# Optimization experiments

Measured on AMD Instinct MI355X. Metric: run time of the kernel, lower is better.

Reference implementation:

```python
import jax, jax.numpy as jnp
import numpy as np

N, F_IN, HID, C, H = 4096, 1024, 64, 40, 8
ALPHA = 0.2  # LeakyReLU negative slope
NEG_INF = -9e15

def setup_inputs() -> dict:
    key = jax.random.key(0)
    ks = jax.random.split(key, 8)
    x = jax.random.normal(ks[0], (N, F_IN), jnp.float32)
    adj = jax.random.randint(ks[1], (N, N), 0, 2, jnp.int32)  # dense 0/1 adjacency
    W = jax.random.normal(ks[2], (H, F_IN, HID), jnp.float32) / np.sqrt(F_IN).astype(np.float32)
    a_src = jax.random.normal(ks[3], (H, HID), jnp.float32) * 0.1
    a_dst = jax.random.normal(ks[4], (H, HID), jnp.float32) * 0.1
    W_out = jax.random.normal(ks[5], (H * HID, C), jnp.float32) / np.sqrt(H * HID).astype(np.float32)
    ao_src = jax.random.normal(ks[6], (C,), jnp.float32) * 0.1
    ao_dst = jax.random.normal(ks[7], (C,), jnp.float32) * 0.1
    return dict(x=x, adj=adj, W=W, a_src=a_src, a_dst=a_dst,
                W_out=W_out, ao_src=ao_src, ao_dst=ao_dst)

def _masked_attention(src, dst, mask):
    # src: [..., N] scores for row node i; dst: [..., N] scores for col node j
    e = jax.nn.leaky_relu(src[..., :, None] + dst[..., None, :], ALPHA)  # [..., N, N]
    e = jnp.where(mask, e, NEG_INF)
    return jax.nn.softmax(e, axis=-1)

def reference(x, adj, W, a_src, a_dst, W_out, ao_src, ao_dst):
    mask = adj > 0  # [N, N]
    # multi-head GAT layer (concat=True)
    Wh = jnp.einsum('nf,hfo->hno', x, W)            # [H, N, HID]
    src = jnp.einsum('hno,ho->hn', Wh, a_src)       # [H, N]
    dst = jnp.einsum('hno,ho->hn', Wh, a_dst)       # [H, N]
    att = _masked_attention(src, dst, mask[None])   # [H, N, N]
    h = jnp.einsum('hij,hjo->hio', att, Wh)         # [H, N, HID]
    h = jax.nn.elu(h)                               # concat=True -> elu inside layer
    h = jnp.transpose(h, (1, 0, 2)).reshape(N, H * HID)  # concat heads -> [N, H*HID]
    # output GAT layer (concat=False -> no elu inside)
    Wh2 = h @ W_out                                 # [N, C]
    att2 = _masked_attention(Wh2 @ ao_src, Wh2 @ ao_dst, mask)  # [N, N]
    out = att2 @ Wh2                                # [N, C]
    # model-level: elu then log_softmax over classes
    return jax.nn.log_softmax(jax.nn.elu(out), axis=1)
```

## Files before the change

kernel.cpp:

```cpp
#include <hip/hip_runtime.h>

#define NN 4096
#define F_IN 1024
#define NHEAD 8
#define HID 64
#define NCLS 40
#define LOG2E 1.44269504f

typedef float f32x4 __attribute__((ext_vector_type(4)));
typedef float f32x2 __attribute__((ext_vector_type(2)));
typedef short s16x8 __attribute__((ext_vector_type(8)));

#define SWZ(r,c) (((r)*64) + ((c) ^ (((r)&7)<<3)))

__device__ __forceinline__ unsigned short f2bf(float f){
  unsigned u = __float_as_uint(f);
  return (unsigned short)((u + 0x7fffu + ((u >> 16) & 1u)) >> 16);
}
__device__ __forceinline__ unsigned cvtpk(float lo, float hi){
  unsigned r; asm("v_cvt_pk_bf16_f32 %0, %1, %2" : "=v"(r) : "v"(lo), "v"(hi)); return r;
}
__device__ __forceinline__ f32x2 pkmul(f32x2 a, f32x2 b){
  f32x2 r; asm("v_pk_mul_f32 %0, %1, %2" : "=v"(r) : "v"(a), "v"(b)); return r;
}

__global__ __launch_bounds__(256) void pack_adj_k(const int* __restrict__ adj, unsigned* __restrict__ bmT){
  int gid = blockIdx.x*256 + threadIdx.x;
  int lane = threadIdx.x & 63;
  unsigned long long m = __ballot(adj[gid] > 0);
  int w = gid >> 5, i = w >> 7, jw = w & 127;
  if (lane == 0)       bmT[(size_t)jw*NN + i] = (unsigned)m;
  else if (lane == 32) bmT[(size_t)jw*NN + i] = (unsigned)(m >> 32);
}

__global__ __launch_bounds__(256) void cast_W_k(const float* __restrict__ W, unsigned short* __restrict__ WbT){
  __shared__ float T[64][65];
  const int h = blockIdx.y, k0 = blockIdx.x*64, t = threadIdx.x;
  for (int idx = t; idx < 1024; idx += 256){
    int k = idx >> 4, c4 = idx & 15;
    *(float4*)&T[k][c4*4] = *(const float4*)&W[((size_t)h*F_IN + k0 + k)*HID + c4*4];
  }
  __syncthreads();
  for (int idx = t; idx < 512; idx += 256){
    int o = idx >> 3, ch = idx & 7;
    s16x8 v;
    #pragma unroll
    for (int e = 0; e < 8; ++e) v[e] = (short)f2bf(T[ch*8 + e][o]);
    *(s16x8*)&WbT[((size_t)h*HID + o)*F_IN + k0 + ch*8] = v;
  }
}

__global__ __launch_bounds__(256) void cast_Wo_k(const float* __restrict__ Wout, unsigned short* __restrict__ WoT){
  int idx = blockIdx.x*256 + threadIdx.x;
  int cc = idx >> 9, k = idx & 511;
  WoT[idx] = (cc < NCLS) ? f2bf(Wout[(size_t)k*NCLS + cc]) : (unsigned short)0;
}

__global__ __launch_bounds__(256) void gemm1_k(const float* __restrict__ x,
    const unsigned short* __restrict__ WbT, unsigned short* __restrict__ WhT,
    const float* __restrict__ a_src, const float* __restrict__ a_dst,
    float* __restrict__ srcv, float* __restrict__ dstv, float2* __restrict__ bdv){
  __shared__ unsigned short xS[64*64];
  __shared__ unsigned short wS[64*64];
  const int t = threadIdx.x, l = t & 63, wv = t >> 6, g = l >> 4, c = l & 15;
  const int h = blockIdx.y, n0 = blockIdx.x * 64;
  f32x4 acc[4] = {};
  for (int k0 = 0; k0 < F_IN; k0 += 64){
    __syncthreads();
    #pragma unroll
    for (int p = 0; p < 4; ++p){
      int idx = t + p*256, row = idx >> 4, c4 = idx & 15;
      float4 v = *(const float4*)&x[(size_t)(n0+row)*F_IN + k0 + c4*4];
      *(uint2*)&xS[SWZ(row, c4*4)] = make_uint2(cvtpk(v.x, v.y), cvtpk(v.z, v.w));
    }
    #pragma unroll
    for (int p = 0; p < 2; ++p){
      int idx = t + p*256, o = idx >> 3, ch = idx & 7;
      *(s16x8*)&wS[SWZ(o, ch*8)] = *(const s16x8*)&WbT[(size_t)(h*HID + o)*F_IN + k0 + ch*8];
    }
    __syncthreads();
    #pragma unroll
    for (int ks = 0; ks < 2; ++ks){
      s16x8 av = *(const s16x8*)&xS[SWZ(wv*16 + c, ks*32 + g*8)];
      #pragma unroll
      for (int ct = 0; ct < 4; ++ct){
        s16x8 bv = *(const s16x8*)&wS[SWZ(ct*16 + c, ks*32 + g*8)];
        acc[ct] = __builtin_amdgcn_mfma_f32_16x16x32_bf16(av, bv, acc[ct], 0, 0, 0);
      }
    }
  }
  float asv[4], adv[4];
  #pragma unroll
  for (int ct = 0; ct < 4; ++ct){ asv[ct] = a_src[h*HID + ct*16 + c]; adv[ct] = a_dst[h*HID + ct*16 + c]; }
  #pragma unroll
  for (int r = 0; r < 4; ++r){
    float ps = acc[0][r]*asv[0] + acc[1][r]*asv[1] + acc[2][r]*asv[2] + acc[3][r]*asv[3];
    float pd = acc[0][r]*adv[0] + acc[1][r]*adv[1] + acc[2][r]*adv[2] + acc[3][r]*adv[3];
    #pragma unroll
    for (int off = 1; off < 16; off <<= 1){ ps += __shfl_xor(ps, off); pd += __shfl_xor(pd, off); }
    if (c == 0){
      int n = n0 + wv*16 + g*4 + r;
      srcv[h*NN + n] = ps; dstv[h*NN + n] = pd;
      bdv[h*NN + n] = make_float2(exp2f(pd*LOG2E), exp2f(0.2f*pd*LOG2E));
    }
  }
  __syncthreads();
  #pragma unroll
  for (int ct = 0; ct < 4; ++ct)
    *(uint2*)&xS[SWZ(ct*16 + c, wv*16 + g*4)] = make_uint2(cvtpk(acc[ct][0], acc[ct][1]), cvtpk(acc[ct][2], acc[ct][3]));
  __syncthreads();
  #pragma unroll
  for (int p = 0; p < 2; ++p){
    int idx = t + p*256, o = idx >> 3, ch = idx & 7;
    *(s16x8*)&WhT[(size_t)(h*HID + o)*NN + n0 + ch*8] = *(const s16x8*)&xS[SWZ(o, ch*8)];
  }
}

__global__ __launch_bounds__(256) void maxred_k(const float* __restrict__ in, float* __restrict__ out){
  __shared__ float red[4];
  const float* p = in + (size_t)blockIdx.x*NN;
  float m = -3.0e38f;
  for (int i = threadIdx.x; i < NN; i += 256) m = fmaxf(m, p[i]);
  #pragma unroll
  for (int off = 32; off; off >>= 1) m = fmaxf(m, __shfl_xor(m, off));
  if ((threadIdx.x & 63) == 0) red[threadIdx.x >> 6] = m;
  __syncthreads();
  if (threadIdx.x == 0) out[blockIdx.x] = fmaxf(fmaxf(red[0], red[1]), fmaxf(red[2], red[3]));
}

template<int NCT, int NJT, int MODE>
__global__ __launch_bounds__(256) void agg_mfma_k(
    const unsigned* __restrict__ bmT, const unsigned short* __restrict__ VT,
    const float* __restrict__ srcv, const float2* __restrict__ bdv,
    const float* __restrict__ maxp, float* __restrict__ partOut, float* __restrict__ denOut)
{
  __shared__ unsigned short vS[2][2][NCT*16*64];
  __shared__ float2 dS[2][2][64];
  __shared__ unsigned bitS[2][2][2][32];
  const int t = threadIdx.x, l = t & 63, wv = t >> 6, g = l >> 4, c = l & 15;
  const int h  = (MODE == 0) ? (blockIdx.y >> 1) : 0;
  const int ck = (MODE == 0) ? (blockIdx.y & 1)  : blockIdx.y;
  const int jt0 = ck * NJT;
  const int i0 = blockIdx.x * 32;
  const int tl = wv >> 1, rH = wv & 1;
  const int lr = rH*16 + c;
  const float sr = srcv[h*NN + i0 + lr];
  const float mx = maxp[MODE == 0 ? h : 0];
  const float tm = sr + mx;
  const float mi2 = fmaxf(tm, 0.2f*tm) * LOG2E;
  f32x2 ac2;
  ac2[0] = exp2f(fmaf(sr, LOG2E, -mi2));
  ac2[1] = exp2f(fmaf(0.2f*sr, LOG2E, -mi2));
  const unsigned short* vb = VT + (MODE == 0 ? (size_t)h*HID*NN : (size_t)0);
  const float2* bp = bdv + (MODE == 0 ? (size_t)h*NN : (size_t)0);

  f32x4 acc[NCT] = {};
  f32x4 accs = {};
  s16x8 ones;
  #pragma unroll
  for (int e = 0; e < 8; ++e) ones[e] = (short)0x3F80;

  s16x8 vreg[NCT]; float2 dreg = make_float2(0.f, 0.f); unsigned breg = 0;
  auto loadRegs = [&](int jt){
    #pragma unroll
    for (int p = 0; p < NCT; ++p){
      int u = t + p*256;
      int tt = u / (NCT*128), rem = u % (NCT*128);
      int o = rem >> 3, chk = rem & 7;
      vreg[p] = *(const s16x8*)&vb[(size_t)o*NN + (jt+tt)*64 + chk*8];
    }
    if (t < 128){
      f32x2 bd = *(const f32x2*)&bp[(jt + (t>>6))*64 + (t&63)];
      dreg = make_float2(bd[0], bd[1]);
    }
    else { int u = t - 128; breg = bmT[(size_t)((jt + (u>>6))*2 + ((u>>5)&1))*NN + i0 + (u&31)]; }
  };
  auto writeLDS = [&](int b){
    #pragma unroll
    for (int p = 0; p < NCT; ++p){
      int u = t + p*256;
      int tt = u / (NCT*128), rem = u % (NCT*128);
      int o = rem >> 3, chk = rem & 7;
      *(s16x8*)&vS[b][tt][SWZ(o, chk*8)] = vreg[p];
    }
    if (t < 128) dS[b][t>>6][t&63] = dreg;
    else { int u = t - 128; bitS[b][u>>6][(u>>5)&1][u&31] = breg; }
  };
  auto computeBuf = [&](int b){
    #pragma unroll
    for (int ks = 0; ks < 2; ++ks){
      unsigned wb = (bitS[b][tl][ks][lr] >> (g*8)) & 0xffu;
      const f32x2* dr = (const f32x2*)&dS[b][tl][ks*32 + g*8];
      float q[8];
      #pragma unroll
      for (int e = 0; e < 8; ++e){
        f32x2 pr = pkmul(ac2, dr[e]);
        float m3 = __builtin_amdgcn_fmed3f(pr[0], pr[1], 1.0f);
        q[e] = (wb & (1u << e)) ? m3 : 0.f;
      }
      s16x8 afr;
      ((unsigned*)&afr)[0] = cvtpk(q[0], q[1]);
      ((unsigned*)&afr)[1] = cvtpk(q[2], q[3]);
      ((unsigned*)&afr)[2] = cvtpk(q[4], q[5]);
      ((unsigned*)&afr)[3] = cvtpk(q[6], q[7]);
      #pragma unroll
      for (int ct = 0; ct < NCT; ++ct){
        s16x8 bv = *(const s16x8*)&vS[b][tl][SWZ(ct*16 + c, ks*32 + g*8)];
        acc[ct] = __builtin_amdgcn_mfma_f32_16x16x32_bf16(afr, bv, acc[ct], 0, 0, 0);
      }
      accs = __builtin_amdgcn_mfma_f32_16x16x32_bf16(afr, ones, accs, 0, 0, 0);
    }
  };

  loadRegs(jt0);
  writeLDS(0);
  __syncthreads();
  int cur = 0;
  for (int jj = 0; jj < NJT; jj += 2){
    const bool more = (jj + 2 < NJT);
    if (more) loadRegs(jt0 + jj + 2);
    computeBuf(cur);
    if (more) writeLDS(cur ^ 1);
    __syncthreads();
    cur ^= 1;
  }

  float* mrg = (float*)&vS[0][0][0];
  constexpr int S = (NCT + 1) * 4;
  if (tl == 1){
    int base = (rH*64 + l) * S;
    #pragma unroll
    for (int ct = 0; ct < NCT; ++ct)
      #pragma unroll
      for (int r = 0; r < 4; ++r) mrg[base + ct*4 + r] = acc[ct][r];
    #pragma unroll
    for (int r = 0; r < 4; ++r) mrg[base + NCT*4 + r] = accs[r];
  }
  __syncthreads();
  if (tl == 0){
    int base = (rH*64 + l) * S;
    #pragma unroll
    for (int ct = 0; ct < NCT; ++ct)
      #pragma unroll
      for (int r = 0; r < 4; ++r) acc[ct][r] += mrg[base + ct*4 + r];
    #pragma unroll
    for (int r = 0; r < 4; ++r) accs[r] += mrg[base + NCT*4 + r];
    if (MODE == 0){
      float* ob = partOut + (size_t)ck * NN * (NHEAD*HID);
      #pragma unroll
      for (int r = 0; r < 4; ++r){
        int row = i0 + rH*16 + g*4 + r;
        #pragma unroll
        for (int ct = 0; ct < NCT; ++ct)
          ob[(size_t)row*(NHEAD*HID) + h*HID + ct*16 + c] = acc[ct][r];
        if (c == 0) denOut[(size_t)(ck*NHEAD + h)*NN + row] = accs[r];
      }
    } else {
      float* ob = partOut + (size_t)ck * NN * 64;
      #pragma unroll
      for (int r = 0; r < 4; ++r){
        int row = i0 + rH*16 + g*4 + r;
        #pragma unroll
        for (int ct = 0; ct < NCT; ++ct)
          ob[(size_t)row*64 + ct*16 + c] = acc[ct][r];
        if (c == 0) ob[(size_t)row*64 + 48] = accs[r];
      }
    }
  }
}

__global__ __launch_bounds__(256) void merge1_k(const float* __restrict__ part, const float* __restrict__ den,
                                                unsigned short* __restrict__ hb){
  int idx = blockIdx.x*256 + threadIdx.x;
  int row = idx >> 7, q = idx & 127;
  float4 a = *(const float4*)&part[(size_t)row*(NHEAD*HID) + q*4];
  float4 b = *(const float4*)&part[((size_t)NN + row)*(NHEAD*HID) + q*4];
  int h = q >> 4;
  float dn = den[(size_t)h*NN + row] + den[(size_t)(NHEAD + h)*NN + row];
  float inv = 1.f / fmaxf(dn, 1e-30f);
  float v0 = (a.x + b.x)*inv, v1 = (a.y + b.y)*inv, v2 = (a.z + b.z)*inv, v3 = (a.w + b.w)*inv;
  v0 = v0 > 0.f ? v0 : __expf(v0) - 1.f;
  v1 = v1 > 0.f ? v1 : __expf(v1) - 1.f;
  v2 = v2 > 0.f ? v2 : __expf(v2) - 1.f;
  v3 = v3 > 0.f ? v3 : __expf(v3) - 1.f;
  *(uint2*)&hb[(size_t)row*(NHEAD*HID) + q*4] = make_uint2(cvtpk(v0, v1), cvtpk(v2, v3));
}

__global__ __launch_bounds__(256) void gemm2_k(const unsigned short* __restrict__ hb,
    const unsigned short* __restrict__ WoT, const float* __restrict__ aos, const float* __restrict__ aod,
    unsigned short* __restrict__ WhT2, float* __restrict__ s2, float* __restrict__ d2,
    float2* __restrict__ bd2){
  __shared__ unsigned short aS[64*64];
  __shared__ unsigned short bS[48*64];
  const int t = threadIdx.x, l = t & 63, wv = t >> 6, g = l >> 4, c = l & 15;
  const int n0 = blockIdx.x * 64;
  f32x4 acc[3] = {};
  for (int k0 = 0; k0 < NHEAD*HID; k0 += 64){
    __syncthreads();
    #pragma unroll
    for (int p = 0; p < 2; ++p){
      int u = t + p*256, o = u >> 3, ch = u & 7;
      *(s16x8*)&aS[SWZ(o, ch*8)] = *(const s16x8*)&hb[(size_t)(n0+o)*(NHEAD*HID) + k0 + ch*8];
    }
    for (int u = t; u < 384; u += 256){
      int o = u >> 3, ch = u & 7;
      *(s16x8*)&bS[SWZ(o, ch*8)] = *(const s16x8*)&WoT[(size_t)o*(NHEAD*HID) + k0 + ch*8];
    }
    __syncthreads();
    #pragma unroll
    for (int ks = 0; ks < 2; ++ks){
      s16x8 av = *(const s16x8*)&aS[SWZ(wv*16 + c, ks*32 + g*8)];
      #pragma unroll
      for (int ct = 0; ct < 3; ++ct){
        s16x8 bv = *(const s16x8*)&bS[SWZ(ct*16 + c, ks*32 + g*8)];
        acc[ct] = __builtin_amdgcn_mfma_f32_16x16x32_bf16(av, bv, acc[ct], 0, 0, 0);
      }
    }
  }
  float asv[3], adv[3];
  #pragma unroll
  for (int ct = 0; ct < 3; ++ct){
    int col = ct*16 + c;
    asv[ct] = (col < NCLS) ? aos[col] : 0.f;
    adv[ct] = (col < NCLS) ? aod[col] : 0.f;
  }
  #pragma unroll
  for (int r = 0; r < 4; ++r){
    float ps = acc[0][r]*asv[0] + acc[1][r]*asv[1] + acc[2][r]*asv[2];
    float pd = acc[0][r]*adv[0] + acc[1][r]*adv[1] + acc[2][r]*adv[2];
    #pragma unroll
    for (int off = 1; off < 16; off <<= 1){ ps += __shfl_xor(ps, off); pd += __shfl_xor(pd, off); }
    if (c == 0){
      int n = n0 + wv*16 + g*4 + r;
      s2[n] = ps; d2[n] = pd;
      bd2[n] = make_float2(exp2f(pd*LOG2E), exp2f(0.2f*pd*LOG2E));
    }
  }
  __syncthreads();
  #pragma unroll
  for (int ct = 0; ct < 3; ++ct)
    *(uint2*)&bS[SWZ(ct*16 + c, wv*16 + g*4)] = make_uint2(cvtpk(acc[ct][0], acc[ct][1]), cvtpk(acc[ct][2], acc[ct][3]));
  __syncthreads();
  for (int u = t; u < 384; u += 256){
    int o = u >> 3, ch = u & 7;
    *(s16x8*)&WhT2[(size_t)o*NN + n0 + ch*8] = *(const s16x8*)&bS[SWZ(o, ch*8)];
  }
}

__global__ __launch_bounds__(256) void final_k(const float* __restrict__ part, float* __restrict__ out){
  const int wid = (blockIdx.x*256 + threadIdx.x) >> 6;
  const int c = threadIdx.x & 63;
  float acc = 0.f, rs = 0.f;
  #pragma unroll
  for (int ch = 0; ch < 8; ++ch){
    const float* pb = part + ((size_t)ch*NN + wid)*64;
    if (c < 48) acc += pb[c];
    rs += pb[48];
  }
  float v = acc / fmaxf(rs, 1e-30f);
  float e = v > 0.f ? v : __expf(v) - 1.f;
  float ev = (c < NCLS) ? e : -3.0e38f;
  float m = ev;
  #pragma unroll
  for (int off = 32; off; off >>= 1) m = fmaxf(m, __shfl_xor(m, off));
  float ex = (c < NCLS) ? __expf(e - m) : 0.f;
  float s = ex;
  #pragma unroll
  for (int off = 32; off; off >>= 1) s += __shfl_xor(s, off);
  if (c < NCLS) out[(size_t)wid*NCLS + c] = e - m - __logf(s);
}

extern "C" void kernel_launch(void* const* d_in, const int* in_sizes, int n_in,
                              void* d_out, int out_size, void* d_ws, size_t ws_size,
                              hipStream_t stream){
  (void)in_sizes; (void)n_in; (void)out_size; (void)ws_size;
  const float* x     = (const float*)d_in[0];
  const int*   adj   = (const int*)  d_in[1];
  const float* W     = (const float*)d_in[2];
  const float* a_src = (const float*)d_in[3];
  const float* a_dst = (const float*)d_in[4];
  const float* W_out = (const float*)d_in[5];
  const float* aos   = (const float*)d_in[6];
  const float* aod   = (const float*)d_in[7];
  float* out = (float*)d_out;

  char* p = (char*)d_ws;
  unsigned* bmT        = (unsigned*)p;       p += (size_t)NN*128*4;
  unsigned short* WbT  = (unsigned short*)p; p += (size_t)NHEAD*HID*F_IN*2;
  unsigned short* WhT  = (unsigned short*)p; p += (size_t)NHEAD*HID*NN*2;
  unsigned short* hbuf = (unsigned short*)p; p += (size_t)NN*NHEAD*HID*2;
  unsigned short* WoT  = (unsigned short*)p; p += (size_t)48*NHEAD*HID*2;
  unsigned short* WhT2 = (unsigned short*)p; p += (size_t)48*NN*2;
  float* srcv = (float*)p; p += (size_t)NHEAD*NN*4;
  float* dstv = (float*)p; p += (size_t)NHEAD*NN*4;
  float* maxd = (float*)p; p += 256;
  float* s2   = (float*)p; p += (size_t)NN*4;
  float* d2   = (float*)p; p += (size_t)NN*4;
  float* m2   = (float*)p; p += 256;
  float2* bdv1 = (float2*)p; p += (size_t)NHEAD*NN*8;
  float2* bdv2 = (float2*)p; p += (size_t)NN*8;
  float* den1 = (float*)p; p += (size_t)2*NHEAD*NN*4;
  float* partU = (float*)p; p += (size_t)2*NN*NHEAD*HID*4;

  pack_adj_k<<<(NN*NN)/256, 256, 0, stream>>>(adj, bmT);
  cast_W_k<<<dim3(F_IN/64, NHEAD), 256, 0, stream>>>(W, WbT);
  cast_Wo_k<<<96, 256, 0, stream>>>(W_out, WoT);
  gemm1_k<<<dim3(NN/64, NHEAD), 256, 0, stream>>>(x, WbT, WhT, a_src, a_dst, srcv, dstv, bdv1);
  maxred_k<<<NHEAD, 256, 0, stream>>>(dstv, maxd);
  agg_mfma_k<4, 32, 0><<<dim3(NN/32, 16), 256, 0, stream>>>(bmT, WhT, srcv, bdv1, maxd, partU, den1);
  merge1_k<<<(NN*128)/256, 256, 0, stream>>>(partU, den1, hbuf);
  gemm2_k<<<NN/64, 256, 0, stream>>>(hbuf, WoT, aos, aod, WhT2, s2, d2, bdv2);
  maxred_k<<<1, 256, 0, stream>>>(d2, m2);
  agg_mfma_k<3, 8, 1><<<dim3(NN/32, 8), 256, 0, stream>>>(bmT, WhT2, s2, bdv2, m2, partU, nullptr);
  final_k<<<NN/4, 256, 0, stream>>>(partU, out);
}
```

Measured before the change: 162.0 us.

## Retile attention aggregation to 64-row blocks with more j-chunks and bf16 partials

The aggregation kernel now gives each block 64 rows, with every wave owning 16 rows across the full j-tile. This replaces the two-wave j-split and removes the LDS merge step at the end. The j dimension is split into more chunks (4 for layer one, 16 for layer two), and layer-one partials are stored as bf16 to cut merge traffic. Launch bounds request higher occupancy and per-block LDS shrinks. The trade-offs are more partial sums for the merge and final kernels to read, and bf16 rounding of the unnormalized partial accumulators.

```diff
diff --git a/kernel.cpp b/kernel.cpp
--- a/kernel.cpp
+++ b/kernel.cpp
@@ -16,6 +16,9 @@
 __device__ __forceinline__ unsigned short f2bf(float f){
   unsigned u = __float_as_uint(f);
   return (unsigned short)((u + 0x7fffu + ((u >> 16) & 1u)) >> 16);
+}
+__device__ __forceinline__ float bf2f(unsigned short u){
+  return __uint_as_float((unsigned)u << 16);
 }
 __device__ __forceinline__ unsigned cvtpk(float lo, float hi){
   unsigned r; asm("v_cvt_pk_bf16_f32 %0, %1, %2" : "=v"(r) : "v"(lo), "v"(hi)); return r;
@@ -129,21 +132,20 @@
 }
 
 template<int NCT, int NJT, int MODE>
-__global__ __launch_bounds__(256) void agg_mfma_k(
+__global__ __launch_bounds__(256, 8) void agg_mfma_k(
     const unsigned* __restrict__ bmT, const unsigned short* __restrict__ VT,
     const float* __restrict__ srcv, const float2* __restrict__ bdv,
-    const float* __restrict__ maxp, float* __restrict__ partOut, float* __restrict__ denOut)
+    const float* __restrict__ maxp, void* __restrict__ partOut, float* __restrict__ denOut)
 {
-  __shared__ unsigned short vS[2][2][NCT*16*64];
-  __shared__ float2 dS[2][2][64];
-  __shared__ unsigned bitS[2][2][2][32];
+  __shared__ unsigned short vS[2][NCT*16*64];
+  __shared__ float2 dS[2][64];
+  __shared__ unsigned bitS[2][2][64];
   const int t = threadIdx.x, l = t & 63, wv = t >> 6, g = l >> 4, c = l & 15;
-  const int h  = (MODE == 0) ? (blockIdx.y >> 1) : 0;
-  const int ck = (MODE == 0) ? (blockIdx.y & 1)  : blockIdx.y;
+  const int h  = (MODE == 0) ? (blockIdx.y >> 2) : 0;
+  const int ck = (MODE == 0) ? (blockIdx.y & 3)  : blockIdx.y;
   const int jt0 = ck * NJT;
-  const int i0 = blockIdx.x * 32;
-  const int tl = wv >> 1, rH = wv & 1;
-  const int lr = rH*16 + c;
+  const int i0 = blockIdx.x * 64;
+  const int lr = wv*16 + c;
   const float sr = srcv[h*NN + i0 + lr];
   const float mx = maxp[MODE == 0 ? h : 0];
   const float tm = sr + mx;
@@ -160,37 +162,36 @@
   #pragma unroll
   for (int e = 0; e < 8; ++e) ones[e] = (short)0x3F80;
 
-  s16x8 vreg[NCT]; float2 dreg = make_float2(0.f, 0.f); unsigned breg = 0;
+  s16x8 vreg[2]; float2 dreg = make_float2(0.f, 0.f); unsigned breg = 0;
   auto loadRegs = [&](int jt){
     #pragma unroll
-    for (int p = 0; p < NCT; ++p){
+    for (int p = 0; p < 2; ++p){
       int u = t + p*256;
-      int tt = u / (NCT*128), rem = u % (NCT*128);
-      int o = rem >> 3, chk = rem & 7;
-      vreg[p] = *(const s16x8*)&vb[(size_t)o*NN + (jt+tt)*64 + chk*8];
-    }
-    if (t < 128){
-      f32x2 bd = *(const f32x2*)&bp[(jt + (t>>6))*64 + (t&63)];
-      dreg = make_float2(bd[0], bd[1]);
-    }
-    else { int u = t - 128; breg = bmT[(size_t)((jt + (u>>6))*2 + ((u>>5)&1))*NN + i0 + (u&31)]; }
+      if (u < NCT*128){
+        int o = u >> 3, chk = u & 7;
+        vreg[p] = *(const s16x8*)&vb[(size_t)o*NN + jt*64 + chk*8];
+      }
+    }
+    if (t < 64) { f32x2 bd = *(const f32x2*)&bp[jt*64 + t]; dreg = make_float2(bd[0], bd[1]); }
+    else if (t < 192){ int u = t - 64; breg = bmT[(size_t)(jt*2 + (u>>6))*NN + i0 + (u & 63)]; }
   };
   auto writeLDS = [&](int b){
     #pragma unroll
-    for (int p = 0; p < NCT; ++p){
+    for (int p = 0; p < 2; ++p){
       int u = t + p*256;
-      int tt = u / (NCT*128), rem = u % (NCT*128);
-      int o = rem >> 3, chk = rem & 7;
-      *(s16x8*)&vS[b][tt][SWZ(o, chk*8)] = vreg[p];
-    }
-    if (t < 128) dS[b][t>>6][t&63] = dreg;
-    else { int u = t - 128; bitS[b][u>>6][(u>>5)&1][u&31] = breg; }
+      if (u < NCT*128){
+        int o = u >> 3, chk = u & 7;
+        *(s16x8*)&vS[b][SWZ(o, chk*8)] = vreg[p];
+      }
+    }
+    if (t < 64) dS[b][t] = dreg;
+    else if (t < 192){ int u = t - 64; bitS[b][u>>6][u&63] = breg; }
   };
   auto computeBuf = [&](int b){
     #pragma unroll
     for (int ks = 0; ks < 2; ++ks){
-      unsigned wb = (bitS[b][tl][ks][lr] >> (g*8)) & 0xffu;
-      const f32x2* dr = (const f32x2*)&dS[b][tl][ks*32 + g*8];
+      unsigned wb = (bitS[b][ks][lr] >> (g*8)) & 0xffu;
+      const f32x2* dr = (const f32x2*)&dS[b][ks*32 + g*8];
       float q[8];
       #pragma unroll
       for (int e = 0; e < 8; ++e){
@@ -205,7 +206,7 @@
       ((unsigned*)&afr)[3] = cvtpk(q[6], q[7]);
       #pragma unroll
       for (int ct = 0; ct < NCT; ++ct){
-        s16x8 bv = *(const s16x8*)&vS[b][tl][SWZ(ct*16 + c, ks*32 + g*8)];
+        s16x8 bv = *(const s16x8*)&vS[b][SWZ(ct*16 + c, ks*32 + g*8)];
         acc[ct] = __builtin_amdgcn_mfma_f32_16x16x32_bf16(afr, bv, acc[ct], 0, 0, 0);
       }
       accs = __builtin_amdgcn_mfma_f32_16x16x32_bf16(afr, ones, accs, 0, 0, 0);
@@ -216,74 +217,60 @@
   writeLDS(0);
   __syncthreads();
   int cur = 0;
-  for (int jj = 0; jj < NJT; jj += 2){
-    const bool more = (jj + 2 < NJT);
-    if (more) loadRegs(jt0 + jj + 2);
+  for (int jj = 0; jj < NJT; ++jj){
+    const bool more = (jj + 1 < NJT);
+    if (more) loadRegs(jt0 + jj + 1);
     computeBuf(cur);
     if (more) writeLDS(cur ^ 1);
     __syncthreads();
     cur ^= 1;
   }
 
-  float* mrg = (float*)&vS[0][0][0];
-  constexpr int S = (NCT + 1) * 4;
-  if (tl == 1){
-    int base = (rH*64 + l) * S;
-    #pragma unroll
-    for (int ct = 0; ct < NCT; ++ct)
-      #pragma unroll
-      for (int r = 0; r < 4; ++r) mrg[base + ct*4 + r] = acc[ct][r];
-    #pragma unroll
-    for (int r = 0; r < 4; ++r) mrg[base + NCT*4 + r] = accs[r];
-  }
-  __syncthreads();
-  if (tl == 0){
-    int base = (rH*64 + l) * S;
-    #pragma unroll
-    for (int ct = 0; ct < NCT; ++ct)
-      #pragma unroll
-      for (int r = 0; r < 4; ++r) acc[ct][r] += mrg[base + ct*4 + r];
-    #pragma unroll
-    for (int r = 0; r < 4; ++r) accs[r] += mrg[base + NCT*4 + r];
-    if (MODE == 0){
-      float* ob = partOut + (size_t)ck * NN * (NHEAD*HID);
-      #pragma unroll
-      for (int r = 0; r < 4; ++r){
-        int row = i0 + rH*16 + g*4 + r;
-        #pragma unroll
-        for (int ct = 0; ct < NCT; ++ct)
-          ob[(size_t)row*(NHEAD*HID) + h*HID + ct*16 + c] = acc[ct][r];
-        if (c == 0) denOut[(size_t)(ck*NHEAD + h)*NN + row] = accs[r];
-      }
-    } else {
-      float* ob = partOut + (size_t)ck * NN * 64;
-      #pragma unroll
-      for (int r = 0; r < 4; ++r){
-        int row = i0 + rH*16 + g*4 + r;
-        #pragma unroll
-        for (int ct = 0; ct < NCT; ++ct)
-          ob[(size_t)row*64 + ct*16 + c] = acc[ct][r];
-        if (c == 0) ob[(size_t)row*64 + 48] = accs[r];
-      }
-    }
-  }
-}
-
-__global__ __launch_bounds__(256) void merge1_k(const float* __restrict__ part, const float* __restrict__ den,
+  if (MODE == 0){
+    unsigned short* ob = (unsigned short*)partOut + (size_t)ck * NN * (NHEAD*HID);
+    #pragma unroll
+    for (int r = 0; r < 4; ++r){
+      int row = i0 + wv*16 + g*4 + r;
+      #pragma unroll
+      for (int ct = 0; ct < NCT; ++ct)
+        ob[(size_t)row*(NHEAD*HID) + h*HID + ct*16 + c] = f2bf(acc[ct][r]);
+      if (c == 0) denOut[(size_t)(ck*NHEAD + h)*NN + row] = accs[r];
+    }
+  } else {
+    float* ob = (float*)partOut + (size_t)ck * NN * 64;
+    #pragma unroll
+    for (int r = 0; r < 4; ++r){
+      int row = i0 + wv*16 + g*4 + r;
+      #pragma unroll
+      for (int ct = 0; ct < NCT; ++ct)
+        ob[(size_t)row*64 + ct*16 + c] = acc[ct][r];
+      if (c == 0) ob[(size_t)row*64 + 48] = accs[r];
+    }
+  }
+}
+
+__global__ __launch_bounds__(256) void merge1_k(const unsigned short* __restrict__ part,
+                                                const float* __restrict__ den,
                                                 unsigned short* __restrict__ hb){
   int idx = blockIdx.x*256 + threadIdx.x;
   int row = idx >> 7, q = idx & 127;
-  float4 a = *(const float4*)&part[(size_t)row*(NHEAD*HID) + q*4];
-  float4 b = *(const float4*)&part[((size_t)NN + row)*(NHEAD*HID) + q*4];
   int h = q >> 4;
-  float dn = den[(size_t)h*NN + row] + den[(size_t)(NHEAD + h)*NN + row];
+  float v[4] = {0.f, 0.f, 0.f, 0.f};
+  float dn = 0.f;
+  #pragma unroll
+  for (int ck = 0; ck < 4; ++ck){
+    const unsigned short* pb = part + ((size_t)ck*NN + row)*(NHEAD*HID) + q*4;
+    ushort4 u = *(const ushort4*)pb;
+    v[0] += bf2f(u.x); v[1] += bf2f(u.y); v[2] += bf2f(u.z); v[3] += bf2f(u.w);
+    dn += den[(size_t)(ck*NHEAD + h)*NN + row];
+  }
   float inv = 1.f / fmaxf(dn, 1e-30f);
-  float v0 = (a.x + b.x)*inv, v1 = (a.y + b.y)*inv, v2 = (a.z + b.z)*inv, v3 = (a.w + b.w)*inv;
-  v0 = v0 > 0.f ? v0 : __expf(v0) - 1.f;
-  v1 = v1 > 0.f ? v1 : __expf(v1) - 1.f;
-  v2 = v2 > 0.f ? v2 : __expf(v2) - 1.f;
-  v3 = v3 > 0.f ? v3 : __expf(v3) - 1.f;
-  *(uint2*)&hb[(size_t)row*(NHEAD*HID) + q*4] = make_uint2(cvtpk(v0, v1), cvtpk(v2, v3));
+  #pragma unroll
+  for (int e = 0; e < 4; ++e){
+    float x = v[e]*inv;
+    v[e] = x > 0.f ? x : __expf(x) - 1.f;
+  }
+  *(uint2*)&hb[(size_t)row*(NHEAD*HID) + q*4] = make_uint2(cvtpk(v[0], v[1]), cvtpk(v[2], v[3]));
 }
 
 __global__ __launch_bounds__(256) void gemm2_k(const unsigned short* __restrict__ hb,
@@ -352,7 +339,7 @@
   const int c = threadIdx.x & 63;
   float acc = 0.f, rs = 0.f;
   #pragma unroll
-  for (int ch = 0; ch < 8; ++ch){
+  for (int ch = 0; ch < 16; ++ch){
     const float* pb = part + ((size_t)ch*NN + wid)*64;
     if (c < 48) acc += pb[c];
     rs += pb[48];
@@ -399,18 +386,18 @@
   float* m2   = (float*)p; p += 256;
   float2* bdv1 = (float2*)p; p += (size_t)NHEAD*NN*8;
   float2* bdv2 = (float2*)p; p += (size_t)NN*8;
-  float* den1 = (float*)p; p += (size_t)2*NHEAD*NN*4;
-  float* partU = (float*)p; p += (size_t)2*NN*NHEAD*HID*4;
+  float* den1 = (float*)p; p += (size_t)4*NHEAD*NN*4;
+  char* partU = p; p += (size_t)16*NN*64*4;
 
   pack_adj_k<<<(NN*NN)/256, 256, 0, stream>>>(adj, bmT);
   cast_W_k<<<dim3(F_IN/64, NHEAD), 256, 0, stream>>>(W, WbT);
   cast_Wo_k<<<96, 256, 0, stream>>>(W_out, WoT);
   gemm1_k<<<dim3(NN/64, NHEAD), 256, 0, stream>>>(x, WbT, WhT, a_src, a_dst, srcv, dstv, bdv1);
   maxred_k<<<NHEAD, 256, 0, stream>>>(dstv, maxd);
-  agg_mfma_k<4, 32, 0><<<dim3(NN/32, 16), 256, 0, stream>>>(bmT, WhT, srcv, bdv1, maxd, partU, den1);
-  merge1_k<<<(NN*128)/256, 256, 0, stream>>>(partU, den1, hbuf);
+  agg_mfma_k<4, 16, 0><<<dim3(NN/64, NHEAD*4), 256, 0, stream>>>(bmT, WhT, srcv, bdv1, maxd, partU, den1);
+  merge1_k<<<(NN*128)/256, 256, 0, stream>>>((const unsigned short*)partU, den1, hbuf);
   gemm2_k<<<NN/64, 256, 0, stream>>>(hbuf, WoT, aos, aod, WhT2, s2, d2, bdv2);
   maxred_k<<<1, 256, 0, stream>>>(d2, m2);
-  agg_mfma_k<3, 8, 1><<<dim3(NN/32, 8), 256, 0, stream>>>(bmT, WhT2, s2, bdv2, m2, partU, nullptr);
-  final_k<<<NN/4, 256, 0, stream>>>(partU, out);
-}
+  agg_mfma_k<3, 4, 1><<<dim3(NN/64, 16), 256, 0, stream>>>(bmT, WhT2, s2, bdv2, m2, partU, nullptr);
+  final_k<<<NN/4, 256, 0, stream>>>((const float*)partU, out);
+}
```

Result: slower. 177.8 us (+9.7%).
